# Kernel tuning notes

Hardware: AMD Instinct MI355X
Metric: run time of the kernel (lower is better)

Reference implementation:

```python
import jax, jax.numpy as jnp
import numpy as np

B, N, I, H = 4, 325, 64, 128
LN_EPS = 1e-5

def setup_inputs() -> dict:
    key = jax.random.key(0)
    ks = jax.random.split(key, 20)
    x = jax.random.normal(ks[0], (B, N, I), dtype=jnp.float32)
    # sparse binary adjacency with self-loops (as the module masks adj == 0)
    a = (jax.random.uniform(ks[1], (B, N, N)) < 0.05).astype(jnp.float32)
    adj = jnp.maximum(a, jnp.eye(N, dtype=jnp.float32)[None])
    h = jax.random.normal(ks[2], (B, N, H), dtype=jnp.float32)
    c = jax.random.normal(ks[3], (B, N, H), dtype=jnp.float32)
    def glorot(k, shape):
        fan_in, fan_out = shape[-1], shape[0]
        s = jnp.sqrt(2.0 / (fan_in + fan_out)).astype(jnp.float32)
        return jax.random.normal(k, shape, dtype=jnp.float32) * s
    params = {
        'W_ih': glorot(ks[4], (4 * H, I)),
        'W_hh': glorot(ks[5], (4 * H, H)),
        'b_ih': jnp.zeros((4 * H,), jnp.float32),
        'b_hh': jnp.zeros((4 * H,), jnp.float32),
        'gc_w': glorot(ks[6], (H, H)),
        'gc_b': jnp.zeros((H,), jnp.float32),
        'Ws_w': glorot(ks[7], (H, H)),
        'Ws_b': jnp.zeros((H,), jnp.float32),
        'Wt_w': glorot(ks[8], (H, H)),
        'Wt_b': jnp.zeros((H,), jnp.float32),
        'v': glorot(ks[9], (H, 1)),
        'ln_g': jnp.ones((H,), jnp.float32),
        'ln_b': jnp.zeros((H,), jnp.float32),
        'comb_w': glorot(ks[10], (H, 2 * H)),
        'comb_b': jnp.zeros((H,), jnp.float32),
    }
    return {'x': x, 'adj': adj, 'h': h, 'c': c, **params}


def reference(x, adj, h, c, W_ih, W_hh, b_ih, b_hh, gc_w, gc_b,
              Ws_w, Ws_b, Wt_w, Wt_b, v, ln_g, ln_b, comb_w, comb_b):
    # --- LSTMCell applied per node (PyTorch gate order: i, f, g, o) ---
    gates = (jnp.einsum('bni,gi->bng', x, W_ih) + b_ih
             + jnp.einsum('bnh,gh->bng', h, W_hh) + b_hh)  # [B,N,4H]
    i_g, f_g, g_g, o_g = jnp.split(gates, 4, axis=-1)
    c_lstm = jax.nn.sigmoid(f_g) * c + jax.nn.sigmoid(i_g) * jnp.tanh(g_g)
    h_lstm = jax.nn.sigmoid(o_g) * jnp.tanh(c_lstm)  # [B,N,H]
    # --- Graph convolution: adj @ (h W) + b ---
    support = jnp.einsum('bnh,ho->bno', h_lstm, gc_w)
    h_graph = jnp.einsum('bnm,bmo->bno', adj, support) + gc_b
    # --- Spatial attention (tanh-additive, adjacency-masked softmax) ---
    s = jnp.einsum('bnh,oh->bno', h_graph, Ws_w) + Ws_b  # W_s(x)
    t = jnp.einsum('bnh,oh->bno', h_graph, Wt_w) + Wt_b  # W_t(x)
    # scores[b,i,j] = tanh(s[b,i] + t[b,j]) @ v ; big [B,N,N,H] intermediate
    scores = jnp.einsum('bijh,h->bij',
                        jnp.tanh(s[:, :, None, :] + t[:, None, :, :]),
                        v[:, 0])
    scores = jnp.where(adj == 0, -1e9, scores)
    attn = jax.nn.softmax(scores, axis=-1)
    context = jnp.einsum('bij,bjh->bih', attn, h_graph)
    # --- LayerNorm ---
    mu = jnp.mean(context, axis=-1, keepdims=True)
    var = jnp.var(context, axis=-1, keepdims=True)
    h_att = ln_g * (context - mu) * jax.lax.rsqrt(var + LN_EPS) + ln_b
    # --- Combine ---
    h_comb = jnp.concatenate([h_lstm, h_att], axis=-1)
    h_new = jnp.einsum('bnk,ok->bno', h_comb, comb_w) + comb_b
    return (h_new, c_lstm)
```

## Files before the change

kernel.cpp:

```cpp
#include <hip/hip_runtime.h>

#define B_ 4
#define N_ 325
#define I_ 64
#define H_ 128
#define NODES (B_ * N_)
#define NZMAX 64

typedef unsigned short u16;
typedef unsigned int u32;

__device__ __align__(16) float g_WT   [192 * 512];
__device__ __align__(16) float g_gcw  [128 * 128];
__device__ __align__(16) float g_WsT  [128 * 128];
__device__ __align__(16) float g_WtT  [128 * 128];
__device__ __align__(16) float g_combT[256 * 128];
__device__ float g_bias[512];
__device__ float g_svec[896];

__device__ __align__(16) float g_support[(size_t)NODES * H_];
__device__ __align__(16) float g_h_graph[(size_t)NODES * H_];
__device__ __align__(16) float g_s_buf  [(size_t)NODES * H_];
__device__ __align__(16) float g_t_buf  [(size_t)NODES * H_];
__device__ __align__(16) float g_hl     [(size_t)NODES * H_];
__device__ u16 g_nz [(size_t)NODES * NZMAX];
__device__ int g_nzc[NODES];

__device__ __forceinline__ float bf2f(u16 u) { return __uint_as_float(((u32)u) << 16); }
__device__ __forceinline__ u16 f2bf(float f) {
    u32 u = __float_as_uint(f);
    u += 0x7fffu + ((u >> 16) & 1u);
    return (u16)(u >> 16);
}
__device__ __forceinline__ float ldin(const void* p, size_t i, int f32) {
    return f32 ? ((const float*)p)[i] : bf2f(((const u16*)p)[i]);
}
__device__ __forceinline__ void stout(void* p, size_t i, float v, int f32) {
    if (f32) ((float*)p)[i] = v; else ((u16*)p)[i] = f2bf(v);
}
__device__ __forceinline__ float fast_rcp(float x) { return __builtin_amdgcn_rcpf(x); }
__device__ __forceinline__ float sigm(float x) { return fast_rcp(1.f + __expf(-x)); }
__device__ __forceinline__ float tanh_f(float x) {
    x = fminf(15.f, fmaxf(-15.f, x));
    float e = __expf(2.f * x);
    return (e - 1.f) * fast_rcp(e + 1.f);
}
__device__ __forceinline__ int probe_f32(const void* adj) {
    return ((((const u32*)adj)[0] & 0xFFFFu) != 0x3F80u) ? 1 : 0;
}

__global__ __launch_bounds__(256) void k0_prep(
    const void* __restrict__ W_ih, const void* __restrict__ W_hh,
    const void* __restrict__ b_ih, const void* __restrict__ b_hh,
    const void* __restrict__ gc_w, const void* __restrict__ gc_b,
    const void* __restrict__ Ws_w, const void* __restrict__ Ws_b,
    const void* __restrict__ Wt_w, const void* __restrict__ Wt_b,
    const void* __restrict__ vvec, const void* __restrict__ ln_g,
    const void* __restrict__ ln_b, const void* __restrict__ comb_w,
    const void* __restrict__ comb_b, const void* __restrict__ adj)
{
    const int f32 = probe_f32(adj);
    const int b = blockIdx.x;
    const int t = threadIdx.x;
    if (b < 40) {
        __shared__ float tile[64][65];
        const void* src; float* dst;
        int C, r0, c0, dstStride, dstRowOff;
        if (b < 8)       { src = W_ih;   dst = g_WT;    C = 64;  r0 = b * 64;            c0 = 0;              dstStride = 512; dstRowOff = 0;  }
        else if (b < 24) { int i = b - 8;  src = W_hh;   dst = g_WT;    C = 128; r0 = (i >> 1) * 64; c0 = (i & 1) * 64;  dstStride = 512; dstRowOff = 64; }
        else if (b < 28) { int i = b - 24; src = Ws_w;   dst = g_WsT;   C = 128; r0 = (i >> 1) * 64; c0 = (i & 1) * 64;  dstStride = 128; dstRowOff = 0;  }
        else if (b < 32) { int i = b - 28; src = Wt_w;   dst = g_WtT;   C = 128; r0 = (i >> 1) * 64; c0 = (i & 1) * 64;  dstStride = 128; dstRowOff = 0;  }
        else             { int i = b - 32; src = comb_w; dst = g_combT; C = 256; r0 = (i >> 2) * 64; c0 = (i & 3) * 64;  dstStride = 128; dstRowOff = 0;  }
        const int lane = t & 63, wv = t >> 6;
        for (int rr = wv; rr < 64; rr += 4)
            tile[rr][lane] = ldin(src, (size_t)(r0 + rr) * C + c0 + lane, f32);
        __syncthreads();
        for (int cc = wv; cc < 64; cc += 4)
            dst[(size_t)(dstRowOff + c0 + cc) * dstStride + r0 + lane] = tile[lane][cc];
    } else {
        for (int e = (b - 40) * 256 + t; e < 16384 + 512 + 896; e += 8 * 256) {
            if (e < 16384) { g_gcw[e] = ldin(gc_w, e, f32); }
            else if (e < 16896) {
                const int i = e - 16384;
                g_bias[i] = ldin(b_ih, i, f32) + ldin(b_hh, i, f32);
            } else {
                const int i = e - 16896;
                const int seg = i >> 7, k = i & 127;
                const void* s = (seg == 0) ? gc_b : (seg == 1) ? Ws_b : (seg == 2) ? Wt_b :
                                (seg == 3) ? vvec : (seg == 4) ? ln_g : (seg == 5) ? ln_b : comb_b;
                g_svec[i] = ldin(s, k, f32);
            }
        }
    }
}

__global__ __launch_bounds__(512) void k1_lstm(
    const void* __restrict__ x, const void* __restrict__ h, const void* __restrict__ c,
    const void* __restrict__ adj, void* __restrict__ out)
{
    const int f32 = probe_f32(adj);
    __shared__ __align__(16) float4 xh4[192];
    __shared__ __align__(16) float4 Gt4[512];
    __shared__ __align__(16) float4 hl4[128];
    const int node0 = blockIdx.x * 4;
    const int t = threadIdx.x;

    for (int e = t; e < 768; e += 512) {
        const int n = e / 192, k = e % 192;
        const int node = node0 + n;
        ((float*)&xh4[k])[n] = (k < 64) ? ldin(x, (size_t)node * 64 + k, f32)
                                        : ldin(h, (size_t)node * 128 + (k - 64), f32);
    }
    __syncthreads();

    {
        const int g = t;
        float a0 = 0.f, a1 = 0.f, a2 = 0.f, a3 = 0.f;
        #pragma unroll 8
        for (int k = 0; k < 192; ++k) {
            const float wv = g_WT[(size_t)k * 512 + g];
            const float4 xv = xh4[k];
            a0 = fmaf(xv.x, wv, a0); a1 = fmaf(xv.y, wv, a1);
            a2 = fmaf(xv.z, wv, a2); a3 = fmaf(xv.w, wv, a3);
        }
        const float bias = g_bias[g];
        Gt4[g] = make_float4(a0 + bias, a1 + bias, a2 + bias, a3 + bias);
    }
    __syncthreads();

    {
        const int n = t >> 7, hh = t & 127;
        const int node = node0 + n;
        const float ig = ((const float*)&Gt4[hh])[n];
        const float fg = ((const float*)&Gt4[128 + hh])[n];
        const float gv = ((const float*)&Gt4[256 + hh])[n];
        const float og = ((const float*)&Gt4[384 + hh])[n];
        const float cl = sigm(fg) * ldin(c, (size_t)node * 128 + hh, f32) + sigm(ig) * tanh_f(gv);
        const float hv = sigm(og) * tanh_f(cl);
        stout(out, (size_t)(NODES * H_) + (size_t)node * 128 + hh, cl, f32);
        g_hl[(size_t)node * 128 + hh] = hv;
        ((float*)&hl4[hh])[n] = hv;
    }
    __syncthreads();

    {
        const int o = t & 127, n = t >> 7;
        float acc = 0.f;
        #pragma unroll 8
        for (int k = 0; k < 128; ++k)
            acc = fmaf(((const float*)&hl4[k])[n], g_gcw[(size_t)k * 128 + o], acc);
        g_support[(size_t)(node0 + n) * 128 + o] = acc;
    }
}

__global__ __launch_bounds__(256) void k2_graph(const void* __restrict__ adj)
{
    const int f32 = probe_f32(adj);
    __shared__ __align__(16) float4 hg4[128];
    __shared__ u16 nzi[4][NZMAX];
    __shared__ float nzv[4][NZMAX];
    __shared__ int cnt[4];
    const int node0 = blockIdx.x * 4;
    const int t = threadIdx.x;
    const int lane = t & 63, w = t >> 6;

    if (t < 4) cnt[t] = 0;
    __syncthreads();
    for (int j = lane; j < N_; j += 64) {
        float a = ldin(adj, (size_t)(node0 + w) * N_ + j, f32);
        if (a != 0.f) {
            int p = atomicAdd(&cnt[w], 1);
            if (p < NZMAX) { nzi[w][p] = (u16)j; nzv[w][p] = a; }
        }
    }
    __syncthreads();
    if (t < 4) g_nzc[node0 + t] = min(cnt[t], NZMAX);
    #pragma unroll
    for (int n = 0; n < 4; ++n) {
        const int cnn = min(cnt[n], NZMAX);
        for (int p = t; p < cnn; p += 256) g_nz[(size_t)(node0 + n) * NZMAX + p] = nzi[n][p];
    }

    const int o = t & 127;
    const float gb = g_svec[o];
    #pragma unroll
    for (int ps = 0; ps < 2; ++ps) {
        const int n = (t >> 7) + 2 * ps;
        const int node = node0 + n;
        const int bn = node / N_;
        const int cnn = min(cnt[n], NZMAX);
        float accA = 0.f, accB = 0.f;
        int p = 0;
        for (; p + 1 < cnn; p += 2) {
            accA = fmaf(nzv[n][p],     g_support[((size_t)bn * N_ + nzi[n][p])     * 128 + o], accA);
            accB = fmaf(nzv[n][p + 1], g_support[((size_t)bn * N_ + nzi[n][p + 1]) * 128 + o], accB);
        }
        if (p < cnn)
            accA = fmaf(nzv[n][p], g_support[((size_t)bn * N_ + nzi[n][p]) * 128 + o], accA);
        const float acc = accA + accB + gb;
        g_h_graph[(size_t)node * 128 + o] = acc;
        ((float*)&hg4[o])[n] = acc;
    }
    __syncthreads();

    {
        const int which = t >> 7;
        const float* WT = which ? g_WtT : g_WsT;
        const float bias = g_svec[128 + which * 128 + o];
        float a0 = 0.f, a1 = 0.f, a2 = 0.f, a3 = 0.f;
        #pragma unroll 8
        for (int k = 0; k < 128; ++k) {
            const float wv = WT[(size_t)k * 128 + o];
            const float4 hv = hg4[k];
            a0 = fmaf(hv.x, wv, a0); a1 = fmaf(hv.y, wv, a1);
            a2 = fmaf(hv.z, wv, a2); a3 = fmaf(hv.w, wv, a3);
        }
        float* dst = which ? g_t_buf : g_s_buf;
        dst[(size_t)(node0 + 0) * 128 + o] = a0 + bias;
        dst[(size_t)(node0 + 1) * 128 + o] = a1 + bias;
        dst[(size_t)(node0 + 2) * 128 + o] = a2 + bias;
        dst[(size_t)(node0 + 3) * 128 + o] = a3 + bias;
    }
}

__global__ __launch_bounds__(256) void k3_attn(
    const void* __restrict__ adj, void* __restrict__ out)
{
    const int f32 = probe_f32(adj);
    __shared__ __align__(16) float4 comb4[256];
    __shared__ float s_i[4][H_];
    __shared__ float red[4][H_];
    __shared__ float nzs[4][NZMAX];
    __shared__ u16 nzi[4][NZMAX];
    __shared__ float part[2][4][H_];
    __shared__ float mu_[4], rstd_[4], smv[4];
    __shared__ int cnt[4];
    const int node0 = blockIdx.x * 4;
    const int t = threadIdx.x;
    const int lane = t & 63, w = t >> 6;

    if (t < 4) cnt[t] = g_nzc[node0 + t];
    for (int e = t; e < 512; e += 256) {
        const int n = e >> 7, k = e & 127;
        const int node = node0 + n;
        s_i[n][k] = g_s_buf[(size_t)node * 128 + k];
        ((float*)&comb4[k])[n] = g_hl[(size_t)node * 128 + k];
    }
    __syncthreads();
    #pragma unroll
    for (int n = 0; n < 4; ++n)
        for (int p = t; p < cnt[n]; p += 256) nzi[n][p] = g_nz[(size_t)(node0 + n) * NZMAX + p];
    __syncthreads();

    {
        const int bn = (node0 + w) / N_;
        const int cn = cnt[w];
        const int sl = lane & 31, hf = lane >> 5;
        const float v0 = g_svec[384 + sl],      v1 = g_svec[384 + 32 + sl];
        const float v2 = g_svec[384 + 64 + sl], v3 = g_svec[384 + 96 + sl];
        const float s0 = s_i[w][sl],      s1 = s_i[w][sl + 32];
        const float s2 = s_i[w][sl + 64], s3 = s_i[w][sl + 96];
        for (int base = 0; base < cn; base += 2) {
            const int p = base + hf;
            float a = 0.f;
            if (p < cn) {
                const float* tj = g_t_buf + ((size_t)bn * N_ + nzi[w][p]) * 128;
                a = v0 * tanh_f(s0 + tj[sl])      + v1 * tanh_f(s1 + tj[sl + 32])
                  + v2 * tanh_f(s2 + tj[sl + 64]) + v3 * tanh_f(s3 + tj[sl + 96]);
            }
            a += __shfl_xor(a, 16); a += __shfl_xor(a, 8);
            a += __shfl_xor(a, 4);  a += __shfl_xor(a, 2); a += __shfl_xor(a, 1);
            if (sl == 0 && p < cn) nzs[w][p] = a;
        }
    }
    __syncthreads();

    if (t < 4) {
        const int cn = cnt[t];
        float m = -1e30f;
        for (int p = 0; p < cn; ++p) m = fmaxf(m, nzs[t][p]);
        float ssum = 0.f;
        for (int p = 0; p < cn; ++p) { float e = __expf(nzs[t][p] - m); nzs[t][p] = e; ssum += e; }
        smv[t] = fast_rcp(ssum);
    }
    __syncthreads();

    const int o = t & 127;
    #pragma unroll
    for (int ps = 0; ps < 2; ++ps) {
        const int n = (t >> 7) + 2 * ps;
        const int bn = (node0 + n) / N_;
        const int cn = cnt[n];
        float accA = 0.f, accB = 0.f;
        int p = 0;
        for (; p + 1 < cn; p += 2) {
            accA = fmaf(nzs[n][p],     g_h_graph[((size_t)bn * N_ + nzi[n][p])     * 128 + o], accA);
            accB = fmaf(nzs[n][p + 1], g_h_graph[((size_t)bn * N_ + nzi[n][p + 1]) * 128 + o], accB);
        }
        if (p < cn)
            accA = fmaf(nzs[n][p], g_h_graph[((size_t)bn * N_ + nzi[n][p]) * 128 + o], accA);
        red[n][o] = (accA + accB) * smv[n];
    }
    __syncthreads();

    {
        float x0 = red[w][lane], x1 = red[w][lane + 64];
        float sm = x0 + x1, sq = x0 * x0 + x1 * x1;
        #pragma unroll
        for (int off = 32; off > 0; off >>= 1) {
            sm += __shfl_xor(sm, off);
            sq += __shfl_xor(sq, off);
        }
        if (lane == 0) {
            float mu = sm * (1.f / H_);
            float var = fmaxf(sq * (1.f / H_) - mu * mu, 0.f);
            mu_[w] = mu;
            rstd_[w] = __builtin_amdgcn_rsqf(var + 1e-5f);
        }
    }
    __syncthreads();
    for (int e = t; e < 512; e += 256) {
        const int n = e >> 7, k = e & 127;
        float xn = (red[n][k] - mu_[n]) * rstd_[n];
        ((float*)&comb4[128 + k])[n] = g_svec[512 + k] * xn + g_svec[640 + k];
    }
    __syncthreads();

    {
        const int half = t >> 7;
        float a0 = 0.f, a1 = 0.f, a2 = 0.f, a3 = 0.f;
        const int k0 = half * 128;
        #pragma unroll 8
        for (int kk = 0; kk < 128; ++kk) {
            const float wv = g_combT[(size_t)(k0 + kk) * 128 + o];
            const float4 cv = comb4[k0 + kk];
            a0 = fmaf(cv.x, wv, a0); a1 = fmaf(cv.y, wv, a1);
            a2 = fmaf(cv.z, wv, a2); a3 = fmaf(cv.w, wv, a3);
        }
        part[half][0][o] = a0; part[half][1][o] = a1;
        part[half][2][o] = a2; part[half][3][o] = a3;
    }
    __syncthreads();
    for (int e = t; e < 512; e += 256) {
        const int n = e >> 7, k = e & 127;
        stout(out, (size_t)(node0 + n) * 128 + k,
              part[0][n][k] + part[1][n][k] + g_svec[768 + k], f32);
    }
}

extern "C" void kernel_launch(void* const* d_in, const int* in_sizes, int n_in,
                              void* d_out, int out_size, void* d_ws, size_t ws_size,
                              hipStream_t stream)
{
    (void)in_sizes; (void)n_in; (void)out_size; (void)d_ws; (void)ws_size;
    const void* x      = d_in[0];
    const void* adj    = d_in[1];
    const void* h      = d_in[2];
    const void* c      = d_in[3];
    const void* W_ih   = d_in[4];
    const void* W_hh   = d_in[5];
    const void* b_ih   = d_in[6];
    const void* b_hh   = d_in[7];
    const void* gc_w   = d_in[8];
    const void* gc_b   = d_in[9];
    const void* Ws_w   = d_in[10];
    const void* Ws_b   = d_in[11];
    const void* Wt_w   = d_in[12];
    const void* Wt_b   = d_in[13];
    const void* vvec   = d_in[14];
    const void* ln_g   = d_in[15];
    const void* ln_b   = d_in[16];
    const void* comb_w = d_in[17];
    const void* comb_b = d_in[18];

    k0_prep <<<48, 256, 0, stream>>>(W_ih, W_hh, b_ih, b_hh, gc_w, gc_b,
                                     Ws_w, Ws_b, Wt_w, Wt_b, vvec, ln_g, ln_b,
                                     comb_w, comb_b, adj);
    k1_lstm <<<NODES / 4, 512, 0, stream>>>(x, h, c, adj, d_out);
    k2_graph<<<NODES / 4, 256, 0, stream>>>(adj);
    k3_attn <<<NODES / 4, 256, 0, stream>>>(adj, d_out);
}
```

Before: 151.6 us.

## Fold weight-prep kernel into LSTM kernel and stage LSTM weights through LDS

Removes the separate weight-transpose prep launch. LSTM blocks now read W_ih/W_hh directly from the inputs in 32-row chunks, transposing into LDS. gc_w and the biases are read directly, and 17 extra blocks in the same grid handle the remaining transposes (Ws, Wt, comb) and small vectors. This saves a kernel launch and the round trip through global memory. In exchange every LSTM block re-reads the full gate weights with strided per-thread loads, and it adds a large 64KB LDS buffer that may lower occupancy.

```diff
diff --git a/kernel.cpp b/kernel.cpp
--- a/kernel.cpp
+++ b/kernel.cpp
@@ -6,16 +6,15 @@
 #define H_ 128
 #define NODES (B_ * N_)
 #define NZMAX 64
+#define LSTMB 325
+#define K1GRID (LSTMB + 17)
 
 typedef unsigned short u16;
 typedef unsigned int u32;
 
-__device__ __align__(16) float g_WT   [192 * 512];
-__device__ __align__(16) float g_gcw  [128 * 128];
 __device__ __align__(16) float g_WsT  [128 * 128];
 __device__ __align__(16) float g_WtT  [128 * 128];
 __device__ __align__(16) float g_combT[256 * 128];
-__device__ float g_bias[512];
 __device__ float g_svec[896];
 
 __device__ __align__(16) float g_support[(size_t)NODES * H_];
@@ -27,6 +26,8 @@
 __device__ int g_nzc[NODES];
 
 __device__ __forceinline__ float bf2f(u16 u) { return __uint_as_float(((u32)u) << 16); }
+__device__ __forceinline__ float lo16(u32 u) { return __uint_as_float(u << 16); }
+__device__ __forceinline__ float hi16(u32 u) { return __uint_as_float(u & 0xffff0000u); }
 __device__ __forceinline__ u16 f2bf(float f) {
     u32 u = __float_as_uint(f);
     u += 0x7fffu + ((u >> 16) & 1u);
@@ -49,7 +50,8 @@
     return ((((const u32*)adj)[0] & 0xFFFFu) != 0x3F80u) ? 1 : 0;
 }
 
-__global__ __launch_bounds__(256) void k0_prep(
+__global__ __launch_bounds__(512) void k1_lstm(
+    const void* __restrict__ x, const void* __restrict__ h, const void* __restrict__ c,
     const void* __restrict__ W_ih, const void* __restrict__ W_hh,
     const void* __restrict__ b_ih, const void* __restrict__ b_hh,
     const void* __restrict__ gc_w, const void* __restrict__ gc_b,
@@ -57,53 +59,42 @@
     const void* __restrict__ Wt_w, const void* __restrict__ Wt_b,
     const void* __restrict__ vvec, const void* __restrict__ ln_g,
     const void* __restrict__ ln_b, const void* __restrict__ comb_w,
-    const void* __restrict__ comb_b, const void* __restrict__ adj)
+    const void* __restrict__ comb_b, const void* __restrict__ adj,
+    void* __restrict__ out)
 {
     const int f32 = probe_f32(adj);
-    const int b = blockIdx.x;
-    const int t = threadIdx.x;
-    if (b < 40) {
-        __shared__ float tile[64][65];
-        const void* src; float* dst;
-        int C, r0, c0, dstStride, dstRowOff;
-        if (b < 8)       { src = W_ih;   dst = g_WT;    C = 64;  r0 = b * 64;            c0 = 0;              dstStride = 512; dstRowOff = 0;  }
-        else if (b < 24) { int i = b - 8;  src = W_hh;   dst = g_WT;    C = 128; r0 = (i >> 1) * 64; c0 = (i & 1) * 64;  dstStride = 512; dstRowOff = 64; }
-        else if (b < 28) { int i = b - 24; src = Ws_w;   dst = g_WsT;   C = 128; r0 = (i >> 1) * 64; c0 = (i & 1) * 64;  dstStride = 128; dstRowOff = 0;  }
-        else if (b < 32) { int i = b - 28; src = Wt_w;   dst = g_WtT;   C = 128; r0 = (i >> 1) * 64; c0 = (i & 1) * 64;  dstStride = 128; dstRowOff = 0;  }
-        else             { int i = b - 32; src = comb_w; dst = g_combT; C = 256; r0 = (i >> 2) * 64; c0 = (i & 3) * 64;  dstStride = 128; dstRowOff = 0;  }
-        const int lane = t & 63, wv = t >> 6;
-        for (int rr = wv; rr < 64; rr += 4)
-            tile[rr][lane] = ldin(src, (size_t)(r0 + rr) * C + c0 + lane, f32);
-        __syncthreads();
-        for (int cc = wv; cc < 64; cc += 4)
-            dst[(size_t)(dstRowOff + c0 + cc) * dstStride + r0 + lane] = tile[lane][cc];
-    } else {
-        for (int e = (b - 40) * 256 + t; e < 16384 + 512 + 896; e += 8 * 256) {
-            if (e < 16384) { g_gcw[e] = ldin(gc_w, e, f32); }
-            else if (e < 16896) {
-                const int i = e - 16384;
-                g_bias[i] = ldin(b_ih, i, f32) + ldin(b_hh, i, f32);
-            } else {
-                const int i = e - 16896;
-                const int seg = i >> 7, k = i & 127;
-                const void* s = (seg == 0) ? gc_b : (seg == 1) ? Ws_b : (seg == 2) ? Wt_b :
-                                (seg == 3) ? vvec : (seg == 4) ? ln_g : (seg == 5) ? ln_b : comb_b;
-                g_svec[i] = ldin(s, k, f32);
-            }
-        }
-    }
-}
-
-__global__ __launch_bounds__(512) void k1_lstm(
-    const void* __restrict__ x, const void* __restrict__ h, const void* __restrict__ c,
-    const void* __restrict__ adj, void* __restrict__ out)
-{
-    const int f32 = probe_f32(adj);
+    __shared__ float WTs[32][513];
     __shared__ __align__(16) float4 xh4[192];
     __shared__ __align__(16) float4 Gt4[512];
     __shared__ __align__(16) float4 hl4[128];
+    const int t = threadIdx.x;
+
+    if (blockIdx.x >= LSTMB) {
+        const int b2 = blockIdx.x - LSTMB;
+        if (b2 < 16) {
+            float (*tile)[65] = reinterpret_cast<float (*)[65]>(&WTs[0][0]);
+            const void* src; float* dst; int C, r0, c0;
+            if (b2 < 4)       { src = Ws_w;   dst = g_WsT;   C = 128; r0 = (b2 >> 1) * 64;        c0 = (b2 & 1) * 64; }
+            else if (b2 < 8)  { int i = b2 - 4; src = Wt_w;   dst = g_WtT;   C = 128; r0 = (i >> 1) * 64; c0 = (i & 1) * 64; }
+            else              { int i = b2 - 8; src = comb_w; dst = g_combT; C = 256; r0 = (i >> 2) * 64; c0 = (i & 3) * 64; }
+            const int lane = t & 63, wv = t >> 6;
+            for (int rr = wv; rr < 64; rr += 8)
+                tile[rr][lane] = ldin(src, (size_t)(r0 + rr) * C + c0 + lane, f32);
+            __syncthreads();
+            for (int cc = wv; cc < 64; cc += 8)
+                dst[(size_t)(c0 + cc) * 128 + r0 + lane] = tile[lane][cc];
+        } else {
+            for (int e = t; e < 896; e += 512) {
+                const int seg = e >> 7, k = e & 127;
+                const void* s = (seg == 0) ? gc_b : (seg == 1) ? Ws_b : (seg == 2) ? Wt_b :
+                                (seg == 3) ? vvec : (seg == 4) ? ln_g : (seg == 5) ? ln_b : comb_b;
+                g_svec[e] = ldin(s, k, f32);
+            }
+        }
+        return;
+    }
+
     const int node0 = blockIdx.x * 4;
-    const int t = threadIdx.x;
 
     for (int e = t; e < 768; e += 512) {
         const int n = e / 192, k = e % 192;
@@ -111,20 +102,42 @@
         ((float*)&xh4[k])[n] = (k < 64) ? ldin(x, (size_t)node * 64 + k, f32)
                                         : ldin(h, (size_t)node * 128 + (k - 64), f32);
     }
-    __syncthreads();
-
-    {
-        const int g = t;
-        float a0 = 0.f, a1 = 0.f, a2 = 0.f, a3 = 0.f;
-        #pragma unroll 8
-        for (int k = 0; k < 192; ++k) {
-            const float wv = g_WT[(size_t)k * 512 + g];
-            const float4 xv = xh4[k];
+
+    float a0 = 0.f, a1 = 0.f, a2 = 0.f, a3 = 0.f;
+    for (int cch = 0; cch < 6; ++cch) {
+        const int k0 = cch * 32;
+        __syncthreads();
+        if (f32) {
+            const float* src = (cch < 2) ? ((const float*)W_ih + (size_t)t * 64 + k0)
+                                         : ((const float*)W_hh + (size_t)t * 128 + (k0 - 64));
+            #pragma unroll
+            for (int j = 0; j < 16; ++j) {
+                const float2 v = ((const float2*)src)[j];
+                WTs[j * 2][t]     = v.x;
+                WTs[j * 2 + 1][t] = v.y;
+            }
+        } else {
+            const u16* src = (cch < 2) ? ((const u16*)W_ih + (size_t)t * 64 + k0)
+                                       : ((const u16*)W_hh + (size_t)t * 128 + (k0 - 64));
+            #pragma unroll
+            for (int j = 0; j < 8; ++j) {
+                const uint2 v = ((const uint2*)src)[j];
+                WTs[j * 4 + 0][t] = lo16(v.x); WTs[j * 4 + 1][t] = hi16(v.x);
+                WTs[j * 4 + 2][t] = lo16(v.y); WTs[j * 4 + 3][t] = hi16(v.y);
+            }
+        }
+        __syncthreads();
+        #pragma unroll
+        for (int kk = 0; kk < 32; ++kk) {
+            const float wv = WTs[kk][t];
+            const float4 xv = xh4[k0 + kk];
             a0 = fmaf(xv.x, wv, a0); a1 = fmaf(xv.y, wv, a1);
             a2 = fmaf(xv.z, wv, a2); a3 = fmaf(xv.w, wv, a3);
         }
-        const float bias = g_bias[g];
-        Gt4[g] = make_float4(a0 + bias, a1 + bias, a2 + bias, a3 + bias);
+    }
+    {
+        const float bias = ldin(b_ih, t, f32) + ldin(b_hh, t, f32);
+        Gt4[t] = make_float4(a0 + bias, a1 + bias, a2 + bias, a3 + bias);
     }
     __syncthreads();
 
@@ -146,9 +159,17 @@
     {
         const int o = t & 127, n = t >> 7;
         float acc = 0.f;
-        #pragma unroll 8
-        for (int k = 0; k < 128; ++k)
-            acc = fmaf(((const float*)&hl4[k])[n], g_gcw[(size_t)k * 128 + o], acc);
+        if (f32) {
+            const float* G = (const float*)gc_w;
+            #pragma unroll 8
+            for (int k = 0; k < 128; ++k)
+                acc = fmaf(((const float*)&hl4[k])[n], G[(size_t)k * 128 + o], acc);
+        } else {
+            const u16* G = (const u16*)gc_w;
+            #pragma unroll 8
+            for (int k = 0; k < 128; ++k)
+                acc = fmaf(((const float*)&hl4[k])[n], bf2f(G[(size_t)k * 128 + o]), acc);
+        }
         g_support[(size_t)(node0 + n) * 128 + o] = acc;
     }
 }
@@ -373,10 +394,10 @@
     const void* comb_w = d_in[17];
     const void* comb_b = d_in[18];
 
-    k0_prep <<<48, 256, 0, stream>>>(W_ih, W_hh, b_ih, b_hh, gc_w, gc_b,
-                                     Ws_w, Ws_b, Wt_w, Wt_b, vvec, ln_g, ln_b,
-                                     comb_w, comb_b, adj);
-    k1_lstm <<<NODES / 4, 512, 0, stream>>>(x, h, c, adj, d_out);
+    k1_lstm <<<K1GRID, 512, 0, stream>>>(x, h, c, W_ih, W_hh, b_ih, b_hh,
+                                         gc_w, gc_b, Ws_w, Ws_b, Wt_w, Wt_b,
+                                         vvec, ln_g, ln_b, comb_w, comb_b,
+                                         adj, d_out);
     k2_graph<<<NODES / 4, 256, 0, stream>>>(adj);
     k3_attn <<<NODES / 4, 256, 0, stream>>>(adj, d_out);
 }
```

Result: slower. 156.4 us (+3.2%).
